# Performance work log

Measured on AMD Instinct MI355X. Metric: run time of the kernel, lower is better.

The kernel has to match this reference:

```python
import jax, jax.numpy as jnp
import numpy as np

N, D, OUT, K = 100000, 256, 128, 10
N1, B = 40960, 4096


def setup_inputs() -> dict:
    key = jax.random.key(0)
    k1, k2, k3, k4, k5, k6, k7 = jax.random.split(key, 7)
    raw_features = jax.random.normal(k1, (N, D), dtype=jnp.float32)
    # xavier-ish init for SageLayer weights [out, 2*in]
    W1 = jax.random.normal(k2, (OUT, 2 * D), dtype=jnp.float32) * (2.0 / (OUT + 2 * D)) ** 0.5
    W2 = jax.random.normal(k3, (OUT, 2 * OUT), dtype=jnp.float32) * (2.0 / (OUT + 2 * OUT)) ** 0.5
    nodes1 = jax.random.randint(k4, (N1,), 0, N)              # layer-1 node ids into raw table
    neighs1 = jax.random.randint(k5, (N1, K), 0, N)           # sampled neighbors (ids into raw table)
    map2 = jax.random.randint(k6, (B,), 0, N1)                # self-index of batch nodes into layer-1 rows
    neighs2 = jax.random.randint(k7, (B, K), 0, N1)           # sampled neighbors (rows of layer-1 embs)
    return {"raw_features": raw_features, "W1": W1, "W2": W2,
            "nodes1": nodes1, "neighs1": neighs1, "map2": map2, "neighs2": neighs2}


def reference(raw_features, W1, W2, nodes1, neighs1, map2, neighs2):
    # Layer 1: mean-aggregate sampled neighbor features (= mask.div(num_neigh).mm(embed_matrix))
    agg1 = jnp.mean(raw_features[neighs1], axis=1)                      # [N1, D]
    self1 = raw_features[nodes1]                                        # [N1, D]
    h1 = jax.nn.relu(jnp.concatenate([self1, agg1], axis=1) @ W1.T)     # [N1, OUT]
    # Layer 2
    agg2 = jnp.mean(h1[neighs2], axis=1)                                # [B, OUT]
    self2 = h1[map2]                                                    # [B, OUT]
    h2 = jax.nn.relu(jnp.concatenate([self2, agg2], axis=1) @ W2.T)     # [B, OUT]
    return h2
```

## Files before the change

### kernel.cpp

```cpp
#include <hip/hip_runtime.h>
#include <hip/hip_bf16.h>

#define N_RAW  100000
#define DIM    256
#define OUTD   128
#define KN     10
#define N1N    40960
#define BATCH  4096
#define SNP    6250
#define SNQ    2560

typedef __attribute__((ext_vector_type(8))) short bf16x8;
typedef __attribute__((ext_vector_type(4))) float f32x4;
typedef __attribute__((ext_vector_type(4))) unsigned int u32x4;
typedef unsigned int u32;

static __device__ inline float b2f(short s) {
  unsigned u = ((unsigned)(unsigned short)s) << 16;
  return __builtin_bit_cast(float, u);
}
static __device__ inline short f2b(float f) {
  unsigned u = __builtin_bit_cast(unsigned, f);
  unsigned r = (u + 0x7fff + ((u >> 16) & 1)) >> 16;
  return (short)r;
}
static __device__ inline u32 cvtpk(float lo, float hi) {
  u32 r;
  asm("v_cvt_pk_bf16_f32 %0, %1, %2" : "=v"(r) : "v"(lo), "v"(hi));
  return r;
}
static __device__ inline void gload_lds16(const void* g, void* l) {
  __builtin_amdgcn_global_load_lds((const __attribute__((address_space(1))) u32*)g,
                                   (__attribute__((address_space(3))) u32*)l, 16, 0, 0);
}

__global__ void build_wc(const float* __restrict__ W1, const float* __restrict__ W2,
                         short* __restrict__ W1c, short* __restrict__ W2c) {
  int i = blockIdx.x * blockDim.x + threadIdx.x;
  {
    int j = i >> 8, k = i & 255;
    float v = (j < OUTD) ? W1[j * (2 * DIM) + k] : W1[(j - OUTD) * (2 * DIM) + DIM + k];
    u32 byte = (u32)((j >> 6) * 32768 + (k >> 6) * 8192 + (j & 63) * 128)
             + (((u32)(2 * (k & 63))) ^ ((u32)(j & 7) << 4));
    *(short*)((char*)W1c + byte) = f2b(v);
  }
  if (i < 256 * 128) {
    int j = i >> 7, k = i & 127;
    float v = (j < OUTD) ? W2[j * (2 * OUTD) + k] : W2[(j - OUTD) * (2 * OUTD) + OUTD + k];
    u32 byte = (u32)((j >> 6) * 16384 + (k >> 6) * 8192 + (j & 63) * 128)
             + (((u32)(2 * (k & 63))) ^ ((u32)(j & 7) << 4));
    *(short*)((char*)W2c + byte) = f2b(v);
  }
}

__global__ __launch_bounds__(512, 8)
void gemm_P(const float* __restrict__ raw, const short* __restrict__ W1c,
            short* __restrict__ P) {
  __shared__ char Blds[32768];
  const int tid  = threadIdx.x;
  const int wave = tid >> 6, lane = tid & 63;
  const int r16  = lane & 15, kg = lane >> 4;
  const int q    = blockIdx.x & 3;
  const int sg   = blockIdx.x >> 2;
  const u32 swz  = (u32)(r16 & 7) << 4;

#pragma unroll
  for (int it = 0; it < 4; ++it)
    gload_lds16((const char*)W1c + q * 32768 + it * 8192 + wave * 1024 + lane * 16,
                Blds + it * 8192 + wave * 1024);
  __syncthreads();

  const int s = sg * 8 + wave;
  if (s >= SNP) return;

  const float* x = raw + (size_t)(s * 16 + r16) * DIM + kg * 8;

  f32x4 acc[4];
#pragma unroll
  for (int n = 0; n < 4; ++n) acc[n] = (f32x4){0.f, 0.f, 0.f, 0.f};

#pragma unroll
  for (int p = 0; p < 4; ++p) {
    f32x4 v0 = *(const f32x4*)(x + p * 64);
    f32x4 v1 = *(const f32x4*)(x + p * 64 + 4);
    f32x4 v2 = *(const f32x4*)(x + p * 64 + 32);
    f32x4 v3 = *(const f32x4*)(x + p * 64 + 36);

    u32x4 t0, t1;
    t0[0] = cvtpk(v0[0], v0[1]); t0[1] = cvtpk(v0[2], v0[3]);
    t0[2] = cvtpk(v1[0], v1[1]); t0[3] = cvtpk(v1[2], v1[3]);
    t1[0] = cvtpk(v2[0], v2[1]); t1[1] = cvtpk(v2[2], v2[3]);
    t1[2] = cvtpk(v3[0], v3[1]); t1[3] = cvtpk(v3[2], v3[3]);
    bf16x8 ab0 = __builtin_bit_cast(bf16x8, t0);
    bf16x8 ab1 = __builtin_bit_cast(bf16x8, t1);

#pragma unroll
    for (int n = 0; n < 4; ++n) {
      u32 base = (u32)(p * 8192 + (n * 16 + r16) * 128);
      bf16x8 b0 = *(const bf16x8*)(Blds + base + (((u32)(kg * 16)) ^ swz));
      bf16x8 b1 = *(const bf16x8*)(Blds + base + (((u32)(64 + kg * 16)) ^ swz));
      acc[n] = __builtin_amdgcn_mfma_f32_16x16x32_bf16(ab0, b0, acc[n], 0, 0, 0);
      acc[n] = __builtin_amdgcn_mfma_f32_16x16x32_bf16(ab1, b1, acc[n], 0, 0, 0);
    }
  }

  short* pb = P + (size_t)(s * 16 + kg * 4) * 256 + q * 64 + r16;
#pragma unroll
  for (int n = 0; n < 4; ++n)
#pragma unroll
    for (int j = 0; j < 4; ++j)
      pb[j * 256 + n * 16] = f2b(acc[n][j]);
}

__global__ __launch_bounds__(512, 8)
void gemm_Q(const short* __restrict__ h1, const short* __restrict__ W2c,
            short* __restrict__ Q) {
  __shared__ char Blds[16384];
  const int tid  = threadIdx.x;
  const int wave = tid >> 6, lane = tid & 63;
  const int r16  = lane & 15, kg = lane >> 4;
  const int q    = blockIdx.x & 3;
  const int sg   = blockIdx.x >> 2;
  const u32 swz  = (u32)(r16 & 7) << 4;

#pragma unroll
  for (int it = 0; it < 2; ++it)
    gload_lds16((const char*)W2c + q * 16384 + it * 8192 + wave * 1024 + lane * 16,
                Blds + it * 8192 + wave * 1024);
  __syncthreads();

  const int s = sg * 8 + wave;
  if (s >= SNQ) return;

  const short* x = h1 + (size_t)(s * 16 + r16) * OUTD + kg * 8;
  bf16x8 a0 = *(const bf16x8*)(x);
  bf16x8 a1 = *(const bf16x8*)(x + 32);
  bf16x8 a2 = *(const bf16x8*)(x + 64);
  bf16x8 a3 = *(const bf16x8*)(x + 96);

  f32x4 acc[4];
#pragma unroll
  for (int n = 0; n < 4; ++n) acc[n] = (f32x4){0.f, 0.f, 0.f, 0.f};

#pragma unroll
  for (int n = 0; n < 4; ++n) {
    u32 row = (u32)((n * 16 + r16) * 128);
    bf16x8 b0 = *(const bf16x8*)(Blds + row + (((u32)(kg * 16)) ^ swz));
    bf16x8 b1 = *(const bf16x8*)(Blds + row + (((u32)(64 + kg * 16)) ^ swz));
    bf16x8 b2 = *(const bf16x8*)(Blds + 8192 + row + (((u32)(kg * 16)) ^ swz));
    bf16x8 b3 = *(const bf16x8*)(Blds + 8192 + row + (((u32)(64 + kg * 16)) ^ swz));
    acc[n] = __builtin_amdgcn_mfma_f32_16x16x32_bf16(a0, b0, acc[n], 0, 0, 0);
    acc[n] = __builtin_amdgcn_mfma_f32_16x16x32_bf16(a1, b1, acc[n], 0, 0, 0);
    acc[n] = __builtin_amdgcn_mfma_f32_16x16x32_bf16(a2, b2, acc[n], 0, 0, 0);
    acc[n] = __builtin_amdgcn_mfma_f32_16x16x32_bf16(a3, b3, acc[n], 0, 0, 0);
  }

  short* qb = Q + (size_t)(s * 16 + kg * 4) * 256 + q * 64 + r16;
#pragma unroll
  for (int n = 0; n < 4; ++n)
#pragma unroll
    for (int j = 0; j < 4; ++j)
      qb[j * 256 + n * 16] = f2b(acc[n][j]);
}

__global__ void gather1(const short* __restrict__ P, const int* __restrict__ nodes1,
                        const int* __restrict__ neighs1, short* __restrict__ h1) {
  int g = threadIdx.x >> 4, t = threadIdx.x & 15;
  int row = blockIdx.x * 16 + g;
  int sn = nodes1[row];
  bf16x8 sv = *(const bf16x8*)(P + (size_t)sn * 256 + t * 8);
  float acc[8];
#pragma unroll
  for (int e = 0; e < 8; ++e) acc[e] = 0.f;
#pragma unroll
  for (int k = 0; k < KN; ++k) {
    int nn = neighs1[row * KN + k];
    bf16x8 nv = *(const bf16x8*)(P + (size_t)nn * 256 + 128 + t * 8);
#pragma unroll
    for (int e = 0; e < 8; ++e) acc[e] += b2f(nv[e]);
  }
  bf16x8 o;
#pragma unroll
  for (int e = 0; e < 8; ++e) o[e] = f2b(fmaxf(b2f(sv[e]) + 0.1f * acc[e], 0.f));
  *(bf16x8*)(h1 + (size_t)row * OUTD + t * 8) = o;
}

__global__ void gather2(const short* __restrict__ Q, const int* __restrict__ map2,
                        const int* __restrict__ neighs2, float* __restrict__ out) {
  int g = threadIdx.x >> 4, t = threadIdx.x & 15;
  int row = blockIdx.x * 16 + g;
  int sn = map2[row];
  bf16x8 sv = *(const bf16x8*)(Q + (size_t)sn * 256 + t * 8);
  float acc[8];
#pragma unroll
  for (int e = 0; e < 8; ++e) acc[e] = 0.f;
#pragma unroll
  for (int k = 0; k < KN; ++k) {
    int nn = neighs2[row * KN + k];
    bf16x8 nv = *(const bf16x8*)(Q + (size_t)nn * 256 + 128 + t * 8);
#pragma unroll
    for (int e = 0; e < 8; ++e) acc[e] += b2f(nv[e]);
  }
  float* orow = out + (size_t)row * OUTD + t * 8;
  float4 o0, o1;
  o0.x = fmaxf(b2f(sv[0]) + 0.1f * acc[0], 0.f);
  o0.y = fmaxf(b2f(sv[1]) + 0.1f * acc[1], 0.f);
  o0.z = fmaxf(b2f(sv[2]) + 0.1f * acc[2], 0.f);
  o0.w = fmaxf(b2f(sv[3]) + 0.1f * acc[3], 0.f);
  o1.x = fmaxf(b2f(sv[4]) + 0.1f * acc[4], 0.f);
  o1.y = fmaxf(b2f(sv[5]) + 0.1f * acc[5], 0.f);
  o1.z = fmaxf(b2f(sv[6]) + 0.1f * acc[6], 0.f);
  o1.w = fmaxf(b2f(sv[7]) + 0.1f * acc[7], 0.f);
  *(float4*)orow = o0;
  *(float4*)(orow + 4) = o1;
}

extern "C" void kernel_launch(void* const* d_in, const int* in_sizes, int n_in,
                              void* d_out, int out_size, void* d_ws, size_t ws_size,
                              hipStream_t stream) {
  const float* raw     = (const float*)d_in[0];
  const float* W1      = (const float*)d_in[1];
  const float* W2      = (const float*)d_in[2];
  const int*   nodes1  = (const int*)d_in[3];
  const int*   neighs1 = (const int*)d_in[4];
  const int*   map2    = (const int*)d_in[5];
  const int*   neighs2 = (const int*)d_in[6];
  float* out = (float*)d_out;

  char* ws = (char*)d_ws;
  short* W1c = (short*)(ws);
  short* W2c = (short*)(ws + 131072);
  short* P   = (short*)(ws + 196608);
  short* Q   = (short*)(ws + 196608);
  short* h1  = (short*)(ws + 51396608);

  build_wc<<<256, 256, 0, stream>>>(W1, W2, W1c, W2c);
  gemm_P<<<3128, 512, 0, stream>>>(raw, W1c, P);
  gather1<<<N1N / 16, 256, 0, stream>>>(P, nodes1, neighs1, h1);
  gemm_Q<<<1280, 512, 0, stream>>>(h1, W2c, Q);
  gather2<<<BATCH / 16, 256, 0, stream>>>(Q, map2, neighs2, out);
}
```

Measured before the change: 112.9 us.

## Double block size in projection GEMMs so each block covers two output quarters

The two projection GEMM kernels now launch 1024-thread blocks, and each block stages half of the weight columns (128 outputs) in LDS instead of a quarter. Pairs of waves share each A-row strip across two 64-column quarters, which halves the number of blocks and means each raw feature row is fetched by two blocks instead of four. The cost is double the LDS per block (64KB for gemm_P), which limits how many blocks fit on a CU, and a larger weight fill before the first barrier. The s bound check was removed in gemm_Q, which is safe because the grid exactly covers SNQ.

```diff
diff --git a/kernel.cpp b/kernel.cpp
--- a/kernel.cpp
+++ b/kernel.cpp
@@ -53,24 +53,26 @@
   }
 }
 
-__global__ __launch_bounds__(512, 8)
+__global__ __launch_bounds__(1024, 8)
 void gemm_P(const float* __restrict__ raw, const short* __restrict__ W1c,
             short* __restrict__ P) {
-  __shared__ char Blds[32768];
+  __shared__ char Blds[65536];
   const int tid  = threadIdx.x;
   const int wave = tid >> 6, lane = tid & 63;
   const int r16  = lane & 15, kg = lane >> 4;
-  const int q    = blockIdx.x & 3;
-  const int sg   = blockIdx.x >> 2;
+  const int half = blockIdx.x & 1;
+  const int sg   = blockIdx.x >> 1;
+  const int lq   = wave & 1;
+  const int wsn  = wave >> 1;
   const u32 swz  = (u32)(r16 & 7) << 4;
 
 #pragma unroll
   for (int it = 0; it < 4; ++it)
-    gload_lds16((const char*)W1c + q * 32768 + it * 8192 + wave * 1024 + lane * 16,
-                Blds + it * 8192 + wave * 1024);
+    gload_lds16((const char*)W1c + half * 65536 + it * 16384 + wave * 1024 + lane * 16,
+                Blds + it * 16384 + wave * 1024);
   __syncthreads();
 
-  const int s = sg * 8 + wave;
+  const int s = sg * 8 + wsn;
   if (s >= SNP) return;
 
   const float* x = raw + (size_t)(s * 16 + r16) * DIM + kg * 8;
@@ -96,7 +98,7 @@
 
 #pragma unroll
     for (int n = 0; n < 4; ++n) {
-      u32 base = (u32)(p * 8192 + (n * 16 + r16) * 128);
+      u32 base = (u32)(lq * 32768 + p * 8192 + (n * 16 + r16) * 128);
       bf16x8 b0 = *(const bf16x8*)(Blds + base + (((u32)(kg * 16)) ^ swz));
       bf16x8 b1 = *(const bf16x8*)(Blds + base + (((u32)(64 + kg * 16)) ^ swz));
       acc[n] = __builtin_amdgcn_mfma_f32_16x16x32_bf16(ab0, b0, acc[n], 0, 0, 0);
@@ -104,7 +106,7 @@
     }
   }
 
-  short* pb = P + (size_t)(s * 16 + kg * 4) * 256 + q * 64 + r16;
+  short* pb = P + (size_t)(s * 16 + kg * 4) * 256 + half * 128 + lq * 64 + r16;
 #pragma unroll
   for (int n = 0; n < 4; ++n)
 #pragma unroll
@@ -112,25 +114,26 @@
       pb[j * 256 + n * 16] = f2b(acc[n][j]);
 }
 
-__global__ __launch_bounds__(512, 8)
+__global__ __launch_bounds__(1024, 8)
 void gemm_Q(const short* __restrict__ h1, const short* __restrict__ W2c,
             short* __restrict__ Q) {
-  __shared__ char Blds[16384];
+  __shared__ char Blds[32768];
   const int tid  = threadIdx.x;
   const int wave = tid >> 6, lane = tid & 63;
   const int r16  = lane & 15, kg = lane >> 4;
-  const int q    = blockIdx.x & 3;
-  const int sg   = blockIdx.x >> 2;
+  const int half = blockIdx.x & 1;
+  const int sg   = blockIdx.x >> 1;
+  const int lq   = wave & 1;
+  const int wsn  = wave >> 1;
   const u32 swz  = (u32)(r16 & 7) << 4;
 
 #pragma unroll
   for (int it = 0; it < 2; ++it)
-    gload_lds16((const char*)W2c + q * 16384 + it * 8192 + wave * 1024 + lane * 16,
-                Blds + it * 8192 + wave * 1024);
+    gload_lds16((const char*)W2c + half * 32768 + it * 16384 + wave * 1024 + lane * 16,
+                Blds + it * 16384 + wave * 1024);
   __syncthreads();
 
-  const int s = sg * 8 + wave;
-  if (s >= SNQ) return;
+  const int s = sg * 8 + wsn;
 
   const short* x = h1 + (size_t)(s * 16 + r16) * OUTD + kg * 8;
   bf16x8 a0 = *(const bf16x8*)(x);
@@ -144,18 +147,18 @@
 
 #pragma unroll
   for (int n = 0; n < 4; ++n) {
-    u32 row = (u32)((n * 16 + r16) * 128);
-    bf16x8 b0 = *(const bf16x8*)(Blds + row + (((u32)(kg * 16)) ^ swz));
-    bf16x8 b1 = *(const bf16x8*)(Blds + row + (((u32)(64 + kg * 16)) ^ swz));
-    bf16x8 b2 = *(const bf16x8*)(Blds + 8192 + row + (((u32)(kg * 16)) ^ swz));
-    bf16x8 b3 = *(const bf16x8*)(Blds + 8192 + row + (((u32)(64 + kg * 16)) ^ swz));
+    u32 base = (u32)(lq * 16384 + (n * 16 + r16) * 128);
+    bf16x8 b0 = *(const bf16x8*)(Blds + base + (((u32)(kg * 16)) ^ swz));
+    bf16x8 b1 = *(const bf16x8*)(Blds + base + (((u32)(64 + kg * 16)) ^ swz));
+    bf16x8 b2 = *(const bf16x8*)(Blds + base + 8192 + (((u32)(kg * 16)) ^ swz));
+    bf16x8 b3 = *(const bf16x8*)(Blds + base + 8192 + (((u32)(64 + kg * 16)) ^ swz));
     acc[n] = __builtin_amdgcn_mfma_f32_16x16x32_bf16(a0, b0, acc[n], 0, 0, 0);
     acc[n] = __builtin_amdgcn_mfma_f32_16x16x32_bf16(a1, b1, acc[n], 0, 0, 0);
     acc[n] = __builtin_amdgcn_mfma_f32_16x16x32_bf16(a2, b2, acc[n], 0, 0, 0);
     acc[n] = __builtin_amdgcn_mfma_f32_16x16x32_bf16(a3, b3, acc[n], 0, 0, 0);
   }
 
-  short* qb = Q + (size_t)(s * 16 + kg * 4) * 256 + q * 64 + r16;
+  short* qb = Q + (size_t)(s * 16 + kg * 4) * 256 + half * 128 + lq * 64 + r16;
 #pragma unroll
   for (int n = 0; n < 4; ++n)
 #pragma unroll
@@ -235,8 +238,8 @@
   short* h1  = (short*)(ws + 51396608);
 
   build_wc<<<256, 256, 0, stream>>>(W1, W2, W1c, W2c);
-  gemm_P<<<3128, 512, 0, stream>>>(raw, W1c, P);
+  gemm_P<<<1564, 1024, 0, stream>>>(raw, W1c, P);
   gather1<<<N1N / 16, 256, 0, stream>>>(P, nodes1, neighs1, h1);
-  gemm_Q<<<1280, 512, 0, stream>>>(h1, W2c, Q);
+  gemm_Q<<<640, 1024, 0, stream>>>(h1, W2c, Q);
   gather2<<<BATCH / 16, 256, 0, stream>>>(Q, map2, neighs2, out);
 }
```

Result: faster. 104.3 us (-7.6%).
